# Kernel tuning notes

Measured on AMD Instinct MI355X. Metric: run time of the kernel, lower is better.

Reference implementation:

```python
import jax, jax.numpy as jnp
import numpy as np

B, T, D, H = 2, 2048, 1024, 16
HD = D // H  # 64


def setup_inputs() -> dict:
    key = jax.random.key(0)
    ks = jax.random.split(key, 9)
    w = lambda k, shp: (jax.random.normal(k, shp, jnp.float32) * 0.02)
    return {
        "x": jax.random.normal(ks[0], (B, T, D), jnp.float32),
        "Wq": w(ks[1], (D, D)), "bq": jnp.zeros((D,), jnp.float32),
        "Wk": w(ks[2], (D, D)), "bk": jnp.zeros((D,), jnp.float32),
        "Wv": w(ks[3], (D, D)), "bv": jnp.zeros((D,), jnp.float32),
        "Wo": w(ks[4], (D, D)), "bo": jnp.zeros((D,), jnp.float32),
        "Wqs": w(ks[5], (3, HD)), "bqs": jnp.zeros((3,), jnp.float32),
        "Wks": w(ks[6], (3, HD)), "bks": jnp.zeros((3,), jnp.float32),
        "Wvs": w(ks[7], (3, HD)), "bvs": jnp.zeros((3,), jnp.float32),
        "temp": jnp.float32(1.0),
    }


def reference(x, Wq, bq, Wk, bk, Wv, bv, Wo, bo, Wqs, bqs, Wks, bks, Wvs, bvs, temp):
    Bx, Tx, Dx = x.shape
    # project and split heads: [B,H,T,HD]
    split = lambda y: y.reshape(Bx, Tx, H, HD).transpose(0, 2, 1, 3)
    q = split(x @ Wq.T + bq)
    k = split(x @ Wk.T + bk)
    v = split(x @ Wv.T + bv)
    # STP projections to 3-d: [B,H,T,3]
    q_stp = q @ Wqs.T + bqs
    k3 = k @ Wks.T + bks
    v3 = v @ Wvs.T + bvs
    # cross-product term (note: original's layernormed k_sub/v_sub are dead code)
    cross_kv = jnp.cross(k3, v3, axis=-1)  # [B,H,T,3]
    scores = (jnp.einsum('bhqd,bhkd->bhqk', q, k)
              + jnp.einsum('bhqc,bhkc->bhqk', q_stp, cross_kv)) * temp
    attn = jax.nn.softmax(scores, axis=-1)
    out = jnp.einsum('bhqk,bhkd->bhqd', attn, v)  # [B,H,T,HD]
    out = out.transpose(0, 2, 1, 3).reshape(Bx, Tx, Dx)
    return out @ Wo.T + bo
```

## Files before the change

kernel.cpp:

```cpp
#include <hip/hip_runtime.h>
#include <stdint.h>

typedef unsigned short u16;
typedef unsigned int u32;
typedef __attribute__((ext_vector_type(8))) short bf16x8;
typedef __attribute__((ext_vector_type(4))) float f32x4;

__device__ __forceinline__ u16 f2b(float f) {
    union { float f; u32 u; } t; t.f = f;
    return (u16)((t.u + 0x7FFFu + ((t.u >> 16) & 1u)) >> 16);
}
__device__ __forceinline__ u32 pack2(float a, float b) {
    return (u32)f2b(a) | ((u32)f2b(b) << 16);
}

__device__ __forceinline__ void async_cp16(const u16* g, const u16* lds_base) {
    __builtin_amdgcn_global_load_lds(
        (const __attribute__((address_space(1))) void*)(uintptr_t)g,
        (__attribute__((address_space(3))) void*)(u32)(uintptr_t)lds_base,
        16, 0, 0);
}

__global__ void cast_all_kernel(const float* __restrict__ x,
                                const float* __restrict__ Wq, const float* __restrict__ Wk,
                                const float* __restrict__ Wv, const float* __restrict__ Wo,
                                u16* __restrict__ xb, u16* __restrict__ Wqb, u16* __restrict__ Wkb,
                                u16* __restrict__ Wvb, u16* __restrict__ Wob) {
    int i = blockIdx.x * blockDim.x + threadIdx.x;
    const float* s; u16* d; int off;
    if (i < 1048576) { s = x; d = xb; off = i; }
    else {
        int j = i - 1048576;
        int w = j >> 18; off = j & 262143;
        if (w == 0) { s = Wq; d = Wqb; }
        else if (w == 1) { s = Wk; d = Wkb; }
        else if (w == 2) { s = Wv; d = Wvb; }
        else { s = Wo; d = Wob; }
    }
    float4 f = ((const float4*)s)[off];
    ((uint2*)d)[off] = make_uint2(pack2(f.x, f.y), pack2(f.z, f.w));
}

__global__ __launch_bounds__(256) void gemm_qkv_kernel(
    const u16* __restrict__ xb,
    const u16* __restrict__ Wq, const u16* __restrict__ Wk, const u16* __restrict__ Wv,
    const float* __restrict__ bq, const float* __restrict__ bk, const float* __restrict__ bv,
    const float* __restrict__ Wqs, const float* __restrict__ bqs,
    const float* __restrict__ Wks, const float* __restrict__ bks,
    const float* __restrict__ Wvs, const float* __restrict__ bvs,
    const float* __restrict__ temp_p,
    u16* __restrict__ qe, u16* __restrict__ ke, u16* __restrict__ vT,
    float4* __restrict__ k3b, float4* __restrict__ v3b)
{
    __shared__ __align__(16) u16 As[64 * 32];
    __shared__ __align__(16) u16 Bs[128 * 32];
    const int tid = threadIdx.x;
    const int lane = tid & 63, w = tid >> 6;
    const int wm = w >> 1, wn = w & 1;
    const int l15 = lane & 15, quad = lane >> 4;
    const int M0 = blockIdx.y * 64, N0 = blockIdx.x * 128;
    const int bz = blockIdx.z;

    const u16* W = (bz == 0) ? Wq : (bz == 1) ? Wk : Wv;
    const float* bias = (bz == 0) ? bq : (bz == 1) ? bk : bv;
    const float* Wst = (bz == 0) ? Wqs : (bz == 1) ? Wks : Wvs;
    const float* bst = (bz == 0) ? bqs : (bz == 1) ? bks : bvs;

    f32x4 acc[2][4];
#pragma unroll
    for (int i = 0; i < 2; i++)
#pragma unroll
        for (int j = 0; j < 4; j++) acc[i][j] = (f32x4){0.f, 0.f, 0.f, 0.f};

    int ra = tid >> 2, ca = ((tid & 3) ^ (ra & 3)) * 8;
    const u16* Aga = xb + (size_t)(M0 + ra) * 1024 + ca;
    const u16* Bg0 = W + (size_t)(N0 + ra) * 1024 + ca;
    const u16* Bg1 = W + (size_t)(N0 + ra + 64) * 1024 + ca;
    const u16* Asb = As + (w * 64) * 8;
    const u16* Bs0 = Bs + (w * 64) * 8;
    const u16* Bs1 = Bs + (256 + w * 64) * 8;

    for (int k0 = 0; k0 < 1024; k0 += 32) {
        __syncthreads();
        async_cp16(Aga + k0, Asb);
        async_cp16(Bg0 + k0, Bs0);
        async_cp16(Bg1 + k0, Bs1);
        __syncthreads();

        bf16x8 af[2], bf[4];
#pragma unroll
        for (int mi = 0; mi < 2; mi++)
            af[mi] = *(const bf16x8*)(As + (wm * 32 + mi * 16 + l15) * 32 + ((quad ^ (l15 & 3)) * 8));
#pragma unroll
        for (int ni = 0; ni < 4; ni++)
            bf[ni] = *(const bf16x8*)(Bs + (wn * 64 + ni * 16 + l15) * 32 + ((quad ^ (l15 & 3)) * 8));
#pragma unroll
        for (int mi = 0; mi < 2; mi++)
#pragma unroll
            for (int ni = 0; ni < 4; ni++)
                acc[mi][ni] = __builtin_amdgcn_mfma_f32_16x16x32_bf16(af[mi], bf[ni], acc[mi][ni], 0, 0, 0);
    }

    const float tau = temp_p[0] * 1.44269504088896f;
    const int nb = N0 + wn * 64;
    const int h = nb >> 6;
    float bias_v[4], wst_v[3][4];
#pragma unroll
    for (int ni = 0; ni < 4; ni++) {
        bias_v[ni] = bias[nb + ni * 16 + l15];
#pragma unroll
        for (int c = 0; c < 3; c++) wst_v[c][ni] = Wst[c * 64 + ni * 16 + l15];
    }
    const float bst0 = bst[0], bst1 = bst[1], bst2 = bst[2];

#pragma unroll
    for (int mi = 0; mi < 2; mi++) {
        int m0 = M0 + wm * 32 + mi * 16 + quad * 4;
        int b = m0 >> 11, t0 = m0 & 2047;
        float p0[4], p1[4], p2[4];
#pragma unroll
        for (int r = 0; r < 4; r++) {
            float a0 = 0.f, a1 = 0.f, a2 = 0.f;
#pragma unroll
            for (int ni = 0; ni < 4; ni++) {
                float v = acc[mi][ni][r] + bias_v[ni];
                a0 += v * wst_v[0][ni];
                a1 += v * wst_v[1][ni];
                a2 += v * wst_v[2][ni];
            }
#pragma unroll
            for (int off = 1; off < 16; off <<= 1) {
                a0 += __shfl_xor(a0, off);
                a1 += __shfl_xor(a1, off);
                a2 += __shfl_xor(a2, off);
            }
            p0[r] = a0 + bst0; p1[r] = a1 + bst1; p2[r] = a2 + bst2;
        }

        if (bz == 0) {
#pragma unroll
            for (int r = 0; r < 4; r++) {
                size_t row = (size_t)((b * 16 + h) * 2048 + (t0 + r));
                u16* qer = qe + row * 96;
#pragma unroll
                for (int ni = 0; ni < 4; ni++)
                    qer[ni * 16 + l15] = f2b((acc[mi][ni][r] + bias_v[ni]) * tau);
                if (l15 == 0) {
                    *(u32*)(qer + 64) = pack2(p0[r] * tau, p1[r] * tau);
                    *(u32*)(qer + 66) = (u32)f2b(p2[r] * tau);
                    uint2 z = make_uint2(0u, 0u);
#pragma unroll
                    for (int j = 68; j < 96; j += 4) *(uint2*)(qer + j) = z;
                }
            }
        } else if (bz == 1) {
#pragma unroll
            for (int r = 0; r < 4; r++) {
                size_t row = (size_t)((b * 16 + h) * 2048 + (t0 + r));
                u16* ker = ke + row * 96;
#pragma unroll
                for (int ni = 0; ni < 4; ni++)
                    ker[ni * 16 + l15] = f2b(acc[mi][ni][r] + bias_v[ni]);
                if (l15 == 0)
                    k3b[row] = make_float4(p0[r], p1[r], p2[r], 0.f);
            }
        } else {
#pragma unroll
            for (int ni = 0; ni < 4; ni++) {
                int hd = ni * 16 + l15;
                float v0 = acc[mi][ni][0] + bias_v[ni];
                float v1 = acc[mi][ni][1] + bias_v[ni];
                float v2 = acc[mi][ni][2] + bias_v[ni];
                float v3 = acc[mi][ni][3] + bias_v[ni];
                *(uint2*)(vT + ((size_t)((b * 16 + h) * 64 + hd)) * 2048 + t0) =
                    make_uint2(pack2(v0, v1), pack2(v2, v3));
            }
            if (l15 == 0) {
#pragma unroll
                for (int r = 0; r < 4; r++) {
                    size_t row = (size_t)((b * 16 + h) * 2048 + (t0 + r));
                    v3b[row] = make_float4(p0[r], p1[r], p2[r], 0.f);
                }
            }
        }
    }
}

__global__ void finish_ext_kernel(const float4* __restrict__ k3b, const float4* __restrict__ v3b,
                                  u16* __restrict__ ke)
{
    int row = blockIdx.x * blockDim.x + threadIdx.x;
    if (row >= 2 * 16 * 2048) return;
    float4 k3 = k3b[row];
    float4 v3 = v3b[row];
    float c0 = k3.y * v3.z - k3.z * v3.y;
    float c1 = k3.z * v3.x - k3.x * v3.z;
    float c2 = k3.x * v3.y - k3.y * v3.x;
    u16* ker = ke + (size_t)row * 96;
    *(u32*)(ker + 64) = pack2(c0, c1);
    *(u32*)(ker + 66) = (u32)f2b(c2);
    uint2 z = make_uint2(0u, 0u);
#pragma unroll
    for (int j = 68; j < 96; j += 4) *(uint2*)(ker + j) = z;
}

__global__ __launch_bounds__(256) void gemm_out_kernel(
    const u16* __restrict__ ao, const u16* __restrict__ Wo, const float* __restrict__ bo,
    float* __restrict__ out)
{
    __shared__ __align__(16) u16 As[64 * 32];
    __shared__ __align__(16) u16 Bs[128 * 32];
    const int tid = threadIdx.x;
    const int lane = tid & 63, w = tid >> 6;
    const int wm = w >> 1, wn = w & 1;
    const int l15 = lane & 15, quad = lane >> 4;
    const int M0 = blockIdx.y * 64, N0 = blockIdx.x * 128;

    f32x4 acc[2][4];
#pragma unroll
    for (int i = 0; i < 2; i++)
#pragma unroll
        for (int j = 0; j < 4; j++) acc[i][j] = (f32x4){0.f, 0.f, 0.f, 0.f};

    int ra = tid >> 2, ca = ((tid & 3) ^ (ra & 3)) * 8;
    const u16* Aga = ao + (size_t)(M0 + ra) * 1024 + ca;
    const u16* Bg0 = Wo + (size_t)(N0 + ra) * 1024 + ca;
    const u16* Bg1 = Wo + (size_t)(N0 + ra + 64) * 1024 + ca;
    const u16* Asb = As + (w * 64) * 8;
    const u16* Bs0 = Bs + (w * 64) * 8;
    const u16* Bs1 = Bs + (256 + w * 64) * 8;

    for (int k0 = 0; k0 < 1024; k0 += 32) {
        __syncthreads();
        async_cp16(Aga + k0, Asb);
        async_cp16(Bg0 + k0, Bs0);
        async_cp16(Bg1 + k0, Bs1);
        __syncthreads();

        bf16x8 af[2], bf[4];
#pragma unroll
        for (int mi = 0; mi < 2; mi++)
            af[mi] = *(const bf16x8*)(As + (wm * 32 + mi * 16 + l15) * 32 + ((quad ^ (l15 & 3)) * 8));
#pragma unroll
        for (int ni = 0; ni < 4; ni++)
            bf[ni] = *(const bf16x8*)(Bs + (wn * 64 + ni * 16 + l15) * 32 + ((quad ^ (l15 & 3)) * 8));
#pragma unroll
        for (int mi = 0; mi < 2; mi++)
#pragma unroll
            for (int ni = 0; ni < 4; ni++)
                acc[mi][ni] = __builtin_amdgcn_mfma_f32_16x16x32_bf16(af[mi], bf[ni], acc[mi][ni], 0, 0, 0);
    }

#pragma unroll
    for (int mi = 0; mi < 2; mi++)
#pragma unroll
        for (int ni = 0; ni < 4; ni++) {
            int n = N0 + wn * 64 + ni * 16 + l15;
            float bias_n = bo[n];
            int m0 = M0 + wm * 32 + mi * 16 + quad * 4;
#pragma unroll
            for (int r = 0; r < 4; r++)
                out[(size_t)(m0 + r) * 1024 + n] = acc[mi][ni][r] + bias_n;
        }
}

__global__ __launch_bounds__(256) void attn_kernel(
    const u16* __restrict__ qe, const u16* __restrict__ ke, const u16* __restrict__ vT,
    u16* __restrict__ out)
{
    __shared__ __align__(16) u16 Ks[64 * 128];
    __shared__ __align__(16) u16 Vt[64 * 64];
    __shared__ __align__(16) u16 Ps[128 * 64];

    const int tid = threadIdx.x;
    const int lane = tid & 63, w = tid >> 6;
    const int l15 = lane & 15, quad = lane >> 4;
    const int lsw = l15 & 7;
    const int bh = blockIdx.y;
    const int q0 = blockIdx.x * 128;

    const u16* qeb = qe + (size_t)bh * 2048 * 96;
    const u16* keb = ke + (size_t)bh * 2048 * 96;
    const u16* vTb = vT + (size_t)bh * 64 * 2048;

    bf16x8 bq[2][3];
#pragma unroll
    for (int s = 0; s < 2; s++) {
        const u16* qrow = qeb + (size_t)(q0 + w * 32 + s * 16 + l15) * 96;
#pragma unroll
        for (int ks = 0; ks < 3; ks++) bq[s][ks] = *(const bf16x8*)(qrow + ks * 32 + quad * 8);
    }

    f32x4 O[2][4];
    float l_part[2];
#pragma unroll
    for (int s = 0; s < 2; s++) {
        l_part[s] = 0.f;
#pragma unroll
        for (int dt = 0; dt < 4; dt++) O[s][dt] = (f32x4){0.f, 0.f, 0.f, 0.f};
    }

    const int srow = tid >> 2, spart = tid & 3;
    const int sh = srow & 7;
    u16* Pw[2];
#pragma unroll
    for (int s = 0; s < 2; s++) Pw[s] = Ps + (size_t)(w * 32 + s * 16 + l15) * 64;

    uint4 kx0, kx1, kx2, vx0, vx1;
    {
        const u16* kg = keb + (size_t)srow * 96;
        kx0 = *(const uint4*)(kg + spart * 8);
        kx1 = *(const uint4*)(kg + (spart + 4) * 8);
        kx2 = *(const uint4*)(kg + (spart + 8) * 8);
        const u16* vg = vTb + (size_t)srow * 2048;
        vx0 = *(const uint4*)(vg + spart * 8);
        vx1 = *(const uint4*)(vg + (spart + 4) * 8);
    }

    for (int kb = 0; kb < 2048; kb += 64) {
        __syncthreads();
        *(uint4*)(Ks + srow * 128 + ((spart    ) ^ sh) * 8) = kx0;
        *(uint4*)(Ks + srow * 128 + ((spart + 4) ^ sh) * 8) = kx1;
        *(uint4*)(Ks + srow * 128 + ((spart + 8) ^ sh) * 8) = kx2;
        *(uint4*)(Vt + srow * 64 + ((spart    ) ^ sh) * 8) = vx0;
        *(uint4*)(Vt + srow * 64 + ((spart + 4) ^ sh) * 8) = vx1;
        __syncthreads();

        if (kb + 64 < 2048) {
            const u16* kg = keb + (size_t)(kb + 64 + srow) * 96;
            kx0 = *(const uint4*)(kg + spart * 8);
            kx1 = *(const uint4*)(kg + (spart + 4) * 8);
            kx2 = *(const uint4*)(kg + (spart + 8) * 8);
            const u16* vg = vTb + (size_t)srow * 2048 + (kb + 64);
            vx0 = *(const uint4*)(vg + spart * 8);
            vx1 = *(const uint4*)(vg + (spart + 4) * 8);
        }

        f32x4 S[2][4];
#pragma unroll
        for (int s = 0; s < 2; s++)
#pragma unroll
            for (int nt = 0; nt < 4; nt++) S[s][nt] = (f32x4){0.f, 0.f, 0.f, 0.f};
#pragma unroll
        for (int ks = 0; ks < 3; ks++) {
            bf16x8 ak[4];
#pragma unroll
            for (int nt = 0; nt < 4; nt++)
                ak[nt] = *(const bf16x8*)(Ks + (nt * 16 + l15) * 128 + (((ks * 4 + quad) ^ lsw) & 15) * 8);
#pragma unroll
            for (int s = 0; s < 2; s++)
#pragma unroll
                for (int nt = 0; nt < 4; nt++)
                    S[s][nt] = __builtin_amdgcn_mfma_f32_16x16x32_bf16(ak[nt], bq[s][ks], S[s][nt], 0, 0, 0);
        }

#pragma unroll
        for (int s = 0; s < 2; s++) {
            float sum = 0.f;
#pragma unroll
            for (int nt = 0; nt < 4; nt++)
#pragma unroll
                for (int r = 0; r < 4; r++) {
                    float p = __builtin_amdgcn_exp2f(S[s][nt][r]);
                    S[s][nt][r] = p;
                    sum += p;
                }
            l_part[s] += sum;
#pragma unroll
            for (int nt = 0; nt < 4; nt++) {
                int c = (nt * 2 + (quad >> 1)) ^ lsw;
                *(uint2*)(Pw[s] + c * 8 + (quad & 1) * 4) =
                    make_uint2(pack2(S[s][nt][0], S[s][nt][1]), pack2(S[s][nt][2], S[s][nt][3]));
            }
        }

#pragma unroll
        for (int kk = 0; kk < 2; kk++) {
            bf16x8 av[4];
#pragma unroll
            for (int dt = 0; dt < 4; dt++)
                av[dt] = *(const bf16x8*)(Vt + (dt * 16 + l15) * 64 + ((kk * 4 + quad) ^ lsw) * 8);
#pragma unroll
            for (int s = 0; s < 2; s++) {
                bf16x8 pb = *(const bf16x8*)(Pw[s] + ((kk * 4 + quad) ^ lsw) * 8);
#pragma unroll
                for (int dt = 0; dt < 4; dt++)
                    O[s][dt] = __builtin_amdgcn_mfma_f32_16x16x32_bf16(av[dt], pb, O[s][dt], 0, 0, 0);
            }
        }
    }

    const int b = bh >> 4, h = bh & 15;
#pragma unroll
    for (int s = 0; s < 2; s++) {
        float l = l_part[s];
        l += __shfl_xor(l, 16);
        l += __shfl_xor(l, 32);
        float linv = 1.0f / l;
        int tq = q0 + w * 32 + s * 16 + l15;
#pragma unroll
        for (int dt = 0; dt < 4; dt++) {
            int d = h * 64 + dt * 16 + quad * 4;
            *(uint2*)(out + (size_t)(b * 2048 + tq) * 1024 + d) =
                make_uint2(pack2(O[s][dt][0] * linv, O[s][dt][1] * linv),
                           pack2(O[s][dt][2] * linv, O[s][dt][3] * linv));
        }
    }
}

extern "C" void kernel_launch(void* const* d_in, const int* in_sizes, int n_in,
                              void* d_out, int out_size, void* d_ws, size_t ws_size,
                              hipStream_t stream)
{
    (void)in_sizes; (void)n_in; (void)out_size; (void)ws_size;
    const float* x   = (const float*)d_in[0];
    const float* Wq  = (const float*)d_in[1];
    const float* bq  = (const float*)d_in[2];
    const float* Wk  = (const float*)d_in[3];
    const float* bk  = (const float*)d_in[4];
    const float* Wv  = (const float*)d_in[5];
    const float* bv  = (const float*)d_in[6];
    const float* Wo  = (const float*)d_in[7];
    const float* bo  = (const float*)d_in[8];
    const float* Wqs = (const float*)d_in[9];
    const float* bqs = (const float*)d_in[10];
    const float* Wks = (const float*)d_in[11];
    const float* bks = (const float*)d_in[12];
    const float* Wvs = (const float*)d_in[13];
    const float* bvs = (const float*)d_in[14];
    const float* temp = (const float*)d_in[15];

    char* ws = (char*)d_ws;
    u16* xb  = (u16*)(ws);
    u16* Wqb = (u16*)(ws + 8388608);
    u16* Wkb = (u16*)(ws + 10485760);
    u16* Wvb = (u16*)(ws + 12582912);
    u16* Wob = (u16*)(ws + 14680064);
    u16* qeb = (u16*)(ws + 16777216);
    u16* keb = (u16*)(ws + 29360128);
    u16* vTb = (u16*)(ws + 41943040);
    float4* k3b = (float4*)(ws + 50331648);
    float4* v3b = (float4*)(ws + 51380224);
    u16* aob = (u16*)(ws + 52428800);

    cast_all_kernel<<<8192, 256, 0, stream>>>(x, Wq, Wk, Wv, Wo, xb, Wqb, Wkb, Wvb, Wob);
    gemm_qkv_kernel<<<dim3(8, 64, 3), 256, 0, stream>>>(
        xb, Wqb, Wkb, Wvb, bq, bk, bv, Wqs, bqs, Wks, bks, Wvs, bvs, temp,
        qeb, keb, vTb, k3b, v3b);
    finish_ext_kernel<<<256, 256, 0, stream>>>(k3b, v3b, keb);
    attn_kernel<<<dim3(16, 32), 256, 0, stream>>>(qeb, keb, vTb, aob);
    gemm_out_kernel<<<dim3(8, 64), 256, 0, stream>>>(aob, Wob, bo, (float*)d_out);
}
```

Measured before the change: 243.8 us.

## Double-buffer K/V tiles and split key dimension across warps in attention

The attention kernel now double-buffers the K and V^T tiles in LDS, so only one barrier is needed per key block and the next tile is stored after compute. The warp layout changes from 4 query-warps of 32 rows each to 2 query groups of 64 rows times 2 key halves. Each warp loads half as many K fragments and reuses them across more query rows. The two key-half partial outputs and row sums are combined through LDS at the end. This adds register pressure (O[4][4] per warp) and uses a larger 64KB shared buffer, with a launch bound of 2 blocks per CU.

Result: faster. 233.9 us (-4.1%).

```diff
diff --git a/kernel.cpp b/kernel.cpp
--- a/kernel.cpp
+++ b/kernel.cpp
@@ -264,16 +264,18 @@
         }
 }
 
-__global__ __launch_bounds__(256) void attn_kernel(
+__global__ __launch_bounds__(256, 2) void attn_kernel(
     const u16* __restrict__ qe, const u16* __restrict__ ke, const u16* __restrict__ vT,
     u16* __restrict__ out)
 {
-    __shared__ __align__(16) u16 Ks[64 * 128];
-    __shared__ __align__(16) u16 Vt[64 * 64];
-    __shared__ __align__(16) u16 Ps[128 * 64];
+    __shared__ __align__(16) u16 smem[32768];
+    u16* const KsA = smem;
+    u16* const VtA = smem + 16384;
+    u16* const PsB = smem + 24576;
 
     const int tid = threadIdx.x;
     const int lane = tid & 63, w = tid >> 6;
+    const int kw = w & 1, qw = w >> 1;
     const int l15 = lane & 15, quad = lane >> 4;
     const int lsw = l15 & 7;
     const int bh = blockIdx.y;
@@ -283,18 +285,18 @@
     const u16* keb = ke + (size_t)bh * 2048 * 96;
     const u16* vTb = vT + (size_t)bh * 64 * 2048;
 
-    bf16x8 bq[2][3];
-#pragma unroll
-    for (int s = 0; s < 2; s++) {
-        const u16* qrow = qeb + (size_t)(q0 + w * 32 + s * 16 + l15) * 96;
+    bf16x8 bq[4][3];
+#pragma unroll
+    for (int s = 0; s < 4; s++) {
+        const u16* qrow = qeb + (size_t)(q0 + qw * 64 + s * 16 + l15) * 96;
 #pragma unroll
         for (int ks = 0; ks < 3; ks++) bq[s][ks] = *(const bf16x8*)(qrow + ks * 32 + quad * 8);
     }
 
-    f32x4 O[2][4];
-    float l_part[2];
-#pragma unroll
-    for (int s = 0; s < 2; s++) {
+    f32x4 O[4][4];
+    float l_part[4];
+#pragma unroll
+    for (int s = 0; s < 4; s++) {
         l_part[s] = 0.f;
 #pragma unroll
         for (int dt = 0; dt < 4; dt++) O[s][dt] = (f32x4){0.f, 0.f, 0.f, 0.f};
@@ -302,31 +304,36 @@
 
     const int srow = tid >> 2, spart = tid & 3;
     const int sh = srow & 7;
-    u16* Pw[2];
-#pragma unroll
-    for (int s = 0; s < 2; s++) Pw[s] = Ps + (size_t)(w * 32 + s * 16 + l15) * 64;
-
-    uint4 kx0, kx1, kx2, vx0, vx1;
+    u16* Pw[4];
+#pragma unroll
+    for (int s = 0; s < 4; s++) Pw[s] = PsB + (size_t)(qw * 64 + s * 16 + l15) * 64;
+
     {
         const u16* kg = keb + (size_t)srow * 96;
-        kx0 = *(const uint4*)(kg + spart * 8);
-        kx1 = *(const uint4*)(kg + (spart + 4) * 8);
-        kx2 = *(const uint4*)(kg + (spart + 8) * 8);
+        uint4 a0 = *(const uint4*)(kg + spart * 8);
+        uint4 a1 = *(const uint4*)(kg + (spart + 4) * 8);
+        uint4 a2 = *(const uint4*)(kg + (spart + 8) * 8);
         const u16* vg = vTb + (size_t)srow * 2048;
-        vx0 = *(const uint4*)(vg + spart * 8);
-        vx1 = *(const uint4*)(vg + (spart + 4) * 8);
-    }
-
+        uint4 b0 = *(const uint4*)(vg + spart * 8);
+        uint4 b1 = *(const uint4*)(vg + (spart + 4) * 8);
+        *(uint4*)(KsA + srow * 128 + ((spart    ) ^ sh) * 8) = a0;
+        *(uint4*)(KsA + srow * 128 + ((spart + 4) ^ sh) * 8) = a1;
+        *(uint4*)(KsA + srow * 128 + ((spart + 8) ^ sh) * 8) = a2;
+        *(uint4*)(VtA + srow * 64 + ((spart    ) ^ sh) * 8) = b0;
+        *(uint4*)(VtA + srow * 64 + ((spart + 4) ^ sh) * 8) = b1;
+    }
+    __syncthreads();
+
+    uint4 kx0, kx1, kx2, vx0, vx1;
     for (int kb = 0; kb < 2048; kb += 64) {
-        __syncthreads();
-        *(uint4*)(Ks + srow * 128 + ((spart    ) ^ sh) * 8) = kx0;
-        *(uint4*)(Ks + srow * 128 + ((spart + 4) ^ sh) * 8) = kx1;
-        *(uint4*)(Ks + srow * 128 + ((spart + 8) ^ sh) * 8) = kx2;
-        *(uint4*)(Vt + srow * 64 + ((spart    ) ^ sh) * 8) = vx0;
-        *(uint4*)(Vt + srow * 64 + ((spart + 4) ^ sh) * 8) = vx1;
-        __syncthreads();
-
-        if (kb + 64 < 2048) {
+        const int buf = (kb >> 6) & 1;
+        const u16* Ks = KsA + buf * 8192;
+        const u16* Vt = VtA + buf * 4096;
+        u16* Ksn = KsA + (buf ^ 1) * 8192;
+        u16* Vtn = VtA + (buf ^ 1) * 4096;
+        const bool more = (kb + 64) < 2048;
+
+        if (more) {
             const u16* kg = keb + (size_t)(kb + 64 + srow) * 96;
             kx0 = *(const uint4*)(kg + spart * 8);
             kx1 = *(const uint4*)(kg + (spart + 4) * 8);
@@ -336,29 +343,29 @@
             vx1 = *(const uint4*)(vg + (spart + 4) * 8);
         }
 
-        f32x4 S[2][4];
-#pragma unroll
-        for (int s = 0; s < 2; s++)
-#pragma unroll
-            for (int nt = 0; nt < 4; nt++) S[s][nt] = (f32x4){0.f, 0.f, 0.f, 0.f};
+        f32x4 S[4][2];
+#pragma unroll
+        for (int s = 0; s < 4; s++)
+#pragma unroll
+            for (int nt = 0; nt < 2; nt++) S[s][nt] = (f32x4){0.f, 0.f, 0.f, 0.f};
 #pragma unroll
         for (int ks = 0; ks < 3; ks++) {
-            bf16x8 ak[4];
-#pragma unroll
-            for (int nt = 0; nt < 4; nt++)
-                ak[nt] = *(const bf16x8*)(Ks + (nt * 16 + l15) * 128 + (((ks * 4 + quad) ^ lsw) & 15) * 8);
-#pragma unroll
-            for (int s = 0; s < 2; s++)
-#pragma unroll
-                for (int nt = 0; nt < 4; nt++)
+            bf16x8 ak[2];
+#pragma unroll
+            for (int nt = 0; nt < 2; nt++)
+                ak[nt] = *(const bf16x8*)(Ks + (kw * 32 + nt * 16 + l15) * 128 + (((ks * 4 + quad) ^ lsw) & 15) * 8);
+#pragma unroll
+            for (int s = 0; s < 4; s++)
+#pragma unroll
+                for (int nt = 0; nt < 2; nt++)
                     S[s][nt] = __builtin_amdgcn_mfma_f32_16x16x32_bf16(ak[nt], bq[s][ks], S[s][nt], 0, 0, 0);
         }
 
 #pragma unroll
-        for (int s = 0; s < 2; s++) {
+        for (int s = 0; s < 4; s++) {
             float sum = 0.f;
 #pragma unroll
-            for (int nt = 0; nt < 4; nt++)
+            for (int nt = 0; nt < 2; nt++)
 #pragma unroll
                 for (int r = 0; r < 4; r++) {
                     float p = __builtin_amdgcn_exp2f(S[s][nt][r]);
@@ -367,43 +374,76 @@
                 }
             l_part[s] += sum;
 #pragma unroll
-            for (int nt = 0; nt < 4; nt++) {
-                int c = (nt * 2 + (quad >> 1)) ^ lsw;
+            for (int nt = 0; nt < 2; nt++) {
+                int c = (kw * 4 + nt * 2 + (quad >> 1)) ^ lsw;
                 *(uint2*)(Pw[s] + c * 8 + (quad & 1) * 4) =
                     make_uint2(pack2(S[s][nt][0], S[s][nt][1]), pack2(S[s][nt][2], S[s][nt][3]));
             }
         }
 
-#pragma unroll
-        for (int kk = 0; kk < 2; kk++) {
+        {
             bf16x8 av[4];
 #pragma unroll
             for (int dt = 0; dt < 4; dt++)
-                av[dt] = *(const bf16x8*)(Vt + (dt * 16 + l15) * 64 + ((kk * 4 + quad) ^ lsw) * 8);
-#pragma unroll
-            for (int s = 0; s < 2; s++) {
-                bf16x8 pb = *(const bf16x8*)(Pw[s] + ((kk * 4 + quad) ^ lsw) * 8);
+                av[dt] = *(const bf16x8*)(Vt + (dt * 16 + l15) * 64 + (((kw * 4 + quad) ^ lsw) & 7) * 8);
+#pragma unroll
+            for (int s = 0; s < 4; s++) {
+                bf16x8 pb = *(const bf16x8*)(Pw[s] + (((kw * 4 + quad) ^ lsw) & 7) * 8);
 #pragma unroll
                 for (int dt = 0; dt < 4; dt++)
                     O[s][dt] = __builtin_amdgcn_mfma_f32_16x16x32_bf16(av[dt], pb, O[s][dt], 0, 0, 0);
             }
         }
-    }
-
-    const int b = bh >> 4, h = bh & 15;
-#pragma unroll
-    for (int s = 0; s < 2; s++) {
-        float l = l_part[s];
-        l += __shfl_xor(l, 16);
-        l += __shfl_xor(l, 32);
-        float linv = 1.0f / l;
-        int tq = q0 + w * 32 + s * 16 + l15;
-#pragma unroll
-        for (int dt = 0; dt < 4; dt++) {
-            int d = h * 64 + dt * 16 + quad * 4;
-            *(uint2*)(out + (size_t)(b * 2048 + tq) * 1024 + d) =
-                make_uint2(pack2(O[s][dt][0] * linv, O[s][dt][1] * linv),
-                           pack2(O[s][dt][2] * linv, O[s][dt][3] * linv));
+
+        if (more) {
+            *(uint4*)(Ksn + srow * 128 + ((spart    ) ^ sh) * 8) = kx0;
+            *(uint4*)(Ksn + srow * 128 + ((spart + 4) ^ sh) * 8) = kx1;
+            *(uint4*)(Ksn + srow * 128 + ((spart + 8) ^ sh) * 8) = kx2;
+            *(uint4*)(Vtn + srow * 64 + ((spart    ) ^ sh) * 8) = vx0;
+            *(uint4*)(Vtn + srow * 64 + ((spart + 4) ^ sh) * 8) = vx1;
+        }
+        __syncthreads();
+    }
+
+    float* const Ored = (float*)smem;
+    float* const Lr = (float*)(smem + 20480);
+    if (kw == 1) {
+#pragma unroll
+        for (int s = 0; s < 4; s++) {
+            float l = l_part[s];
+            l += __shfl_xor(l, 16);
+            l += __shfl_xor(l, 32);
+            if (lane < 16) Lr[qw * 64 + s * 16 + l15] = l;
+            int qrow = qw * 64 + s * 16 + l15;
+#pragma unroll
+            for (int dt = 0; dt < 4; dt++) {
+                int dc = dt ^ (l15 & 3);
+                *(float4*)(Ored + qrow * 68 + dc * 16 + quad * 4) =
+                    make_float4(O[s][dt][0], O[s][dt][1], O[s][dt][2], O[s][dt][3]);
+            }
+        }
+    }
+    __syncthreads();
+    if (kw == 0) {
+        const int b = bh >> 4, h = bh & 15;
+#pragma unroll
+        for (int s = 0; s < 4; s++) {
+            float l = l_part[s];
+            l += __shfl_xor(l, 16);
+            l += __shfl_xor(l, 32);
+            int qrow = qw * 64 + s * 16 + l15;
+            l += Lr[qrow];
+            float linv = 1.0f / l;
+            int tq = q0 + qrow;
+#pragma unroll
+            for (int dt = 0; dt < 4; dt++) {
+                int dc = dt ^ (l15 & 3);
+                float4 o2 = *(const float4*)(Ored + qrow * 68 + dc * 16 + quad * 4);
+                int d = h * 64 + dt * 16 + quad * 4;
+                *(uint2*)(out + (size_t)(b * 2048 + tq) * 1024 + d) =
+                    make_uint2(pack2((O[s][dt][0] + o2.x) * linv, (O[s][dt][1] + o2.y) * linv),
+                               pack2((O[s][dt][2] + o2.z) * linv, (O[s][dt][3] + o2.w) * linv));
+            }
         }
     }
 }
```
